# Performance work log

Measured on AMD Instinct MI355X. Metric: run time of the kernel, lower is better.

## Reference

```python
import jax, jax.numpy as jnp
import numpy as np

NUM_HEADS = 16


def setup_inputs() -> dict:
    key = jax.random.key(0)
    ks = jax.random.split(key, 5)
    S, B, N, C = 4, 2, 2048, 1024
    return {
        "x_all": jax.random.normal(ks[0], (S, B, N, C), dtype=jnp.float32),
        "w_qkv": jax.random.normal(ks[1], (C, 3 * C), dtype=jnp.float32) * (C ** -0.5),
        "b_qkv": jax.random.normal(ks[2], (3 * C,), dtype=jnp.float32) * 0.02,
        "w_proj": jax.random.normal(ks[3], (C, C), dtype=jnp.float32) * (C ** -0.5),
        "b_proj": jax.random.normal(ks[4], (C,), dtype=jnp.float32) * 0.02,
    }


def reference(x_all, w_qkv, b_qkv, w_proj, b_proj):
    # x_all: [S, B, N, C] -- S = cp_dim ring shards, each rank holds [B, N, C]
    S, B, N, C = x_all.shape
    H = NUM_HEADS
    D = C // H
    scale = 1.0 / np.sqrt(D).astype(np.float32)

    # same qkv projection on every rank
    qkv = (jnp.einsum("sbnc,ce->sbne", x_all, w_qkv) + b_qkv)
    qkv = qkv.reshape(S, B, N, 3, H, D)
    # rank 0's queries: [B, H, N, D]
    q = jnp.transpose(qkv[0, :, :, 0], (0, 2, 1, 3))
    # all shards' keys/values: [S, B, H, N, D]
    k = jnp.transpose(qkv[:, :, :, 1], (0, 1, 3, 2, 4))
    v = jnp.transpose(qkv[:, :, :, 2], (0, 1, 3, 2, 4))

    # ring loop: online softmax merge across KV shards (numerically stable
    # form of the source's exp(lse)-weighted average)
    attn_out, lse = None, None
    for s in range(S):
        scores = jnp.einsum("bhnd,bhmd->bhnm", q, k[s]) * scale  # [B,H,N,N]
        new_lse = jax.nn.logsumexp(scores, axis=-1)               # [B,H,N]
        probs = jnp.exp(scores - new_lse[..., None])
        new_out = jnp.einsum("bhnm,bhmd->bhnd", probs, v[s])      # [B,H,N,D]
        if attn_out is None:
            attn_out, lse = new_out, new_lse
        else:
            m = jnp.logaddexp(lse, new_lse)
            attn_out = (attn_out * jnp.exp(lse - m)[..., None]
                        + new_out * jnp.exp(new_lse - m)[..., None])
            lse = m

    # [B,H,N,D] -> [B,N,C]
    out = jnp.transpose(attn_out, (0, 2, 1, 3)).reshape(B, N, C)
    return out @ w_proj + b_proj
```

## Files before the change

kernel.cpp:

```cpp
#include <hip/hip_runtime.h>
#include <hip/hip_bf16.h>


typedef __bf16 bf16x8 __attribute__((ext_vector_type(8)));
typedef float v4f __attribute__((ext_vector_type(4)));

#if __has_builtin(__builtin_amdgcn_exp2f)
#define EXP2F(x) __builtin_amdgcn_exp2f(x)
#else
#define EXP2F(x) exp2f(x)
#endif

__device__ __forceinline__ float bf2f(unsigned short h) {
  union { unsigned int u; float f; } a; a.u = ((unsigned int)h) << 16; return a.f;
}
__device__ __forceinline__ unsigned short f2bf(float f) {
  union { float f; unsigned int u; } a; a.f = f;
  unsigned int u = a.u;
  unsigned int r = (u + 0x7fffu + ((u >> 16) & 1u)) >> 16;
  return (unsigned short)r;
}
__device__ __forceinline__ unsigned int pack2t(float a, float b) {
  union { float f; unsigned int u; } ua, ub; ua.f = a; ub.f = b;
  return (ua.u >> 16) | (ub.u & 0xffff0000u);
}
__device__ __forceinline__ bf16x8 ldfrag16(const unsigned short* p) {
  union { uint4 u; bf16x8 v; } x; x.u = *(const uint4*)p; return x.v;
}
__device__ __forceinline__ bf16x8 ones8() {
  union { unsigned short s[8]; bf16x8 v; } x;
#pragma unroll
  for (int i = 0; i < 8; i++) x.s[i] = 0x3F80;
  return x.v;
}
__device__ __forceinline__ void gld_lds16(const unsigned short* g, unsigned short* l) {
  __builtin_amdgcn_global_load_lds((__attribute__((address_space(1))) void*)g,
                                   (__attribute__((address_space(3))) void*)l, 16, 0, 0);
}

__global__ void detect_dtype(const unsigned short* __restrict__ x, int* flag) {
  __shared__ int cnt;
  if (threadIdx.x == 0) cnt = 0;
  __syncthreads();
  int sane = 0;
#pragma unroll
  for (int j = 0; j < 4; j++) {
    unsigned short v = x[2 * (threadIdx.x + 64 * j)];
    int e = (v >> 7) & 0xFF;
    if (e >= 90 && e <= 140) sane++;
  }
  atomicAdd(&cnt, sane);
  __syncthreads();
  if (threadIdx.x == 0) *flag = (cnt > 160) ? 0 : 1;
}

__global__ void conv_to_bf16(const void* __restrict__ in, unsigned short* __restrict__ out,
                             int n4, const int* __restrict__ flag) {
  int i = blockIdx.x * blockDim.x + threadIdx.x;
  if (i >= n4) return;
  if (*flag) {
    float4 v = ((const float4*)in)[i];
    ushort4 o;
    o.x = f2bf(v.x); o.y = f2bf(v.y); o.z = f2bf(v.z); o.w = f2bf(v.w);
    ((ushort4*)out)[i] = o;
  } else {
    ((ushort4*)out)[i] = ((const ushort4*)in)[i];
  }
}

__global__ void conv_bias(const void* __restrict__ bq_in, const void* __restrict__ bp_in,
                          unsigned short* __restrict__ bq, unsigned short* __restrict__ bp,
                          const int* __restrict__ flag) {
  int i = blockIdx.x * 256 + threadIdx.x;
  const void* in = (i < 768) ? bq_in : bp_in;
  unsigned short* out = (i < 768) ? bq : bp;
  int j = (i < 768) ? i : i - 768;
  if (*flag) {
    float4 v = ((const float4*)in)[j];
    ushort4 o;
    o.x = f2bf(v.x); o.y = f2bf(v.y); o.z = f2bf(v.z); o.w = f2bf(v.w);
    ((ushort4*)out)[j] = o;
  } else {
    ((ushort4*)out)[j] = ((const ushort4*)in)[j];
  }
}

__global__ void trans_both(const void* __restrict__ wqkv, const void* __restrict__ wproj,
                           unsigned short* __restrict__ wt1, unsigned short* __restrict__ wt2,
                           const int* __restrict__ flag) {
  __shared__ unsigned short t[32][33];
  int tx = threadIdx.x, ty = threadIdx.y;
  int bx = blockIdx.x;
  const void* in; unsigned short* out; int C, c0;
  if (bx < 96) { in = wqkv; out = wt1; C = 3072; c0 = bx * 32; }
  else         { in = wproj; out = wt2; C = 1024; c0 = (bx - 96) * 32; }
  const int R = 1024;
  int r0 = blockIdx.y * 32;
  int fp = *flag;
#pragma unroll
  for (int j = 0; j < 32; j += 8) {
    unsigned short v;
    if (fp) v = f2bf(((const float*)in)[(r0 + ty + j) * C + c0 + tx]);
    else    v = ((const unsigned short*)in)[(r0 + ty + j) * C + c0 + tx];
    t[ty + j][tx] = v;
  }
  __syncthreads();
#pragma unroll
  for (int j = 0; j < 32; j += 8) out[(c0 + ty + j) * R + r0 + tx] = t[tx][ty + j];
}

template <int MODE>
__launch_bounds__(256, 3)
__global__ void gemm_bt(const unsigned short* __restrict__ A,
                        const unsigned short* __restrict__ Bt,
                        const unsigned short* __restrict__ bias,
                        void* __restrict__ Cout,
                        int K, int ldc, const int* __restrict__ flag,
                        const unsigned short* Bt2, const unsigned short* bias2,
                        void* Cout2,
                        const unsigned short* Bt3, const unsigned short* bias3,
                        void* Cout3) {
  __shared__ unsigned short As[128 * 32];
  __shared__ unsigned short Bs[128 * 32];
  int tid = threadIdx.x;
  int w = tid >> 6, lane = tid & 63, col = lane & 15, quad = lane >> 4;
  int wm = w >> 1, wn = w & 1;
  const unsigned short* Bt_ = Bt;
  const unsigned short* bias_ = bias;
  void* Cout_ = Cout;
  bool isq = false, isv = false;
  int n0, m0;
  if constexpr (MODE == 4) {
    int id = blockIdx.x;
    int xcd = id & 7, t = id >> 3;
    n0 = (t & 7) * 128;
    int y = xcd * 36 + (t >> 3);
    if (y < 256) {
      m0 = (y >> 1) * 128;
      if (y & 1) { isv = true; Bt_ = Bt3; bias_ = bias3; Cout_ = Cout3; }
    } else {
      m0 = (y - 256) * 128;
      isq = true; Bt_ = Bt2; bias_ = bias2; Cout_ = Cout2;
    }
  } else {
    int id = blockIdx.x;
    int xcd = id & 7, t = id >> 3;
    n0 = (t & 7) * 128;
    m0 = (xcd * 4 + (t >> 3)) * 128;
  }
  int fp = 0;
  if constexpr (MODE == 2) fp = *flag;

  v4f acc[4][4];
#pragma unroll
  for (int i = 0; i < 4; i++)
#pragma unroll
    for (int j = 0; j < 4; j++) acc[i][j] = v4f{0.f, 0.f, 0.f, 0.f};

  int ra0 = tid >> 2, cc = tid & 3;
  const unsigned short* ga0 = &A[(m0 + ra0) * K + cc * 8];
  const unsigned short* ga1 = ga0 + 64 * K;
  const unsigned short* gb0 = &Bt_[(n0 + ra0) * K + cc * 8];
  const unsigned short* gb1 = gb0 + 64 * K;
  unsigned short* lA0 = &As[(w * 16) * 32];
  unsigned short* lA1 = &As[(64 + w * 16) * 32];
  unsigned short* lB0 = &Bs[(w * 16) * 32];
  unsigned short* lB1 = &Bs[(64 + w * 16) * 32];

  int niter = K >> 5;
  for (int it = 0; it < niter; it++) {
    __syncthreads();
    gld_lds16(ga0, lA0); gld_lds16(ga1, lA1);
    gld_lds16(gb0, lB0); gld_lds16(gb1, lB1);
    ga0 += 32; ga1 += 32; gb0 += 32; gb1 += 32;
    __syncthreads();
    bf16x8 af[4], bfr[4];
#pragma unroll
    for (int mi = 0; mi < 4; mi++) af[mi] = ldfrag16(&As[(wm * 64 + mi * 16 + col) * 32 + quad * 8]);
#pragma unroll
    for (int ni = 0; ni < 4; ni++) bfr[ni] = ldfrag16(&Bs[(wn * 64 + ni * 16 + col) * 32 + quad * 8]);
#pragma unroll
    for (int mi = 0; mi < 4; mi++)
#pragma unroll
      for (int ni = 0; ni < 4; ni++)
        acc[mi][ni] = __builtin_amdgcn_mfma_f32_16x16x32_bf16(af[mi], bfr[ni], acc[mi][ni], 0, 0, 0);
  }

  float bv[4];
#pragma unroll
  for (int ni = 0; ni < 4; ni++) bv[ni] = bf2f(bias_[n0 + wn * 64 + ni * 16 + col]);

  if (MODE == 4 && isv) {
    int rgb0 = m0 + wm * 64;
    int s = rgb0 >> 12, b = (rgb0 >> 11) & 1, n = rgb0 & 2047;
    int kvg0 = s * 2048 + n;
#pragma unroll
    for (int ni = 0; ni < 4; ni++) {
      int cg = n0 + wn * 64 + ni * 16 + col;
      int h = cg >> 6, d = cg & 63;
      unsigned short* rowp = &((unsigned short*)Cout_)[((b * 16 + h) * 64 + d) * 8192 + kvg0];
      float bvn = bv[ni];
#pragma unroll
      for (int r = 0; r < 4; r++) {
        ushort2 e, o2;
        e.x = f2bf(acc[0][ni][r] + bvn);
        e.y = f2bf(acc[2][ni][r] + bvn);
        o2.x = f2bf(acc[1][ni][r] + bvn);
        o2.y = f2bf(acc[3][ni][r] + bvn);
        *(ushort2*)&rowp[2 * (quad * 4 + r)] = e;
        *(ushort2*)&rowp[32 + 2 * (quad * 4 + r)] = o2;
      }
    }
  } else {
#pragma unroll
    for (int mi = 0; mi < 4; mi++)
#pragma unroll
      for (int ni = 0; ni < 4; ni++) {
        float vals[4];
#pragma unroll
        for (int r = 0; r < 4; r++) vals[r] = acc[mi][ni][r] + bv[ni];
        if constexpr (MODE == 4) {
          if (isq) {
#pragma unroll
            for (int r = 0; r < 4; r++) vals[r] *= 0.1803368801111601f;
          }
        }
        int rgb = m0 + wm * 64 + mi * 16 + quad * 4;
        int cg  = n0 + wn * 64 + ni * 16 + col;
        if constexpr (MODE == 4) {
          unsigned short* C = (unsigned short*)Cout_;
#pragma unroll
          for (int r = 0; r < 4; r++) C[(rgb + r) * ldc + cg] = f2bf(vals[r]);
        } else {
          if (fp) {
            float* C = (float*)Cout_;
#pragma unroll
            for (int r = 0; r < 4; r++) C[(rgb + r) * ldc + cg] = vals[r];
          } else {
            unsigned short* C = (unsigned short*)Cout_;
#pragma unroll
            for (int r = 0; r < 4; r++) C[(rgb + r) * ldc + cg] = f2bf(vals[r]);
          }
        }
      }
  }
}

__launch_bounds__(512, 4)
__global__ void attn_kernel(const unsigned short* __restrict__ qbuf,
                            const unsigned short* __restrict__ kbuf,
                            const unsigned short* __restrict__ vt,
                            float* __restrict__ po,
                            float* __restrict__ lbuf) {
  __shared__ unsigned short Ks[2][64 * 64];
  __shared__ unsigned short Vs[3][64 * 64];
  int tid = threadIdx.x;
  int w = tid >> 6, lane = tid & 63, col = lane & 15, quad = lane >> 4;
  int id = blockIdx.x;
  int xcd = id & 7, slot = id >> 3;
  int qt = slot & 7, gsub = slot >> 3;
  int g = gsub * 8 + xcd;
  int bh = g >> 1, half = g & 1;
  int b = bh >> 4, h = bh & 15;
  int q0 = qt * 256;

  bf16x8 aQ[2][2];
#pragma unroll
  for (int mj = 0; mj < 2; mj++)
#pragma unroll
    for (int kk = 0; kk < 2; kk++)
      aQ[mj][kk] = ldfrag16(&qbuf[(b * 2048 + q0 + w * 32 + mj * 16 + col) * 1024 +
                                  h * 64 + kk * 32 + quad * 8]);

  int r0 = tid >> 3, c0 = tid & 7;
  const unsigned short* kp = &kbuf[((half * 2) * 4096 + b * 2048 + r0) * 1024 + h * 64 + c0 * 8];
  const unsigned short* vp = &vt[(bh * 64 + r0) * 8192 + half * 4096 + c0 * 8];
  int sdst = r0 * 64 + 8 * (c0 ^ (r0 & 7));

  const bf16x8 vone = ones8();
  v4f o[2][4];
  v4f acc_l[2] = {v4f{0.f, 0.f, 0.f, 0.f}, v4f{0.f, 0.f, 0.f, 0.f}};
#pragma unroll
  for (int mj = 0; mj < 2; mj++)
#pragma unroll
    for (int di = 0; di < 4; di++) o[mj][di] = v4f{0.f, 0.f, 0.f, 0.f};

  {
    uint4 k0 = *(const uint4*)kp, v0 = *(const uint4*)vp;
    *(uint4*)&Ks[0][sdst] = k0;
    *(uint4*)&Vs[0][sdst] = v0;
  }
  kp += 64 * 1024; vp += 64;
  uint4 pk = *(const uint4*)kp, pv = *(const uint4*)vp;
  __syncthreads();

  bf16x8 aP[2][2];
  {
    v4f sc[4][2];
#pragma unroll
    for (int ni = 0; ni < 4; ni++)
#pragma unroll
      for (int mj = 0; mj < 2; mj++) sc[ni][mj] = v4f{0.f, 0.f, 0.f, 0.f};
#pragma unroll
    for (int kk = 0; kk < 2; kk++) {
      bf16x8 aK[4];
#pragma unroll
      for (int ni = 0; ni < 4; ni++) {
        int row = ni * 16 + col;
        aK[ni] = ldfrag16(&Ks[0][row * 64 + 8 * ((kk * 4 + quad) ^ (col & 7))]);
      }
#pragma unroll
      for (int ni = 0; ni < 4; ni++)
#pragma unroll
        for (int mj = 0; mj < 2; mj++)
          sc[ni][mj] = __builtin_amdgcn_mfma_f32_16x16x32_bf16(aK[ni], aQ[mj][kk], sc[ni][mj], 0, 0, 0);
    }
#pragma unroll
    for (int ni = 0; ni < 4; ni++)
#pragma unroll
      for (int mj = 0; mj < 2; mj++)
#pragma unroll
        for (int r = 0; r < 4; r++) sc[ni][mj][r] = EXP2F(sc[ni][mj][r]);
#pragma unroll
    for (int mj = 0; mj < 2; mj++)
#pragma unroll
      for (int kk = 0; kk < 2; kk++) {
        union { unsigned int d[4]; bf16x8 v; } u;
#pragma unroll
        for (int t = 0; t < 4; t++)
          u.d[t] = pack2t(sc[kk][mj][t], sc[kk + 2][mj][t]);
        aP[mj][kk] = u.v;
      }
  }
  *(uint4*)&Ks[1][sdst] = pk;
  *(uint4*)&Vs[1][sdst] = pv;
  __syncthreads();

  const unsigned short* vprev = Vs[0];
  const unsigned short* vcur  = Vs[1];
  const unsigned short* vnext = Vs[2];

  for (int t = 1; t < 64; t++) {
    const unsigned short* kcur = Ks[t & 1];
    unsigned short* knxt = (unsigned short*)Ks[(t + 1) & 1];
    if (t < 63) {
      int kstep = (((t + 1) & 31) == 0) ? (2048 + 64) * 1024 : 64 * 1024;
      kp += kstep; vp += 64;
      pk = *(const uint4*)kp; pv = *(const uint4*)vp;
    }

    v4f sc[4][2];
#pragma unroll
    for (int ni = 0; ni < 4; ni++)
#pragma unroll
      for (int mj = 0; mj < 2; mj++) sc[ni][mj] = v4f{0.f, 0.f, 0.f, 0.f};
#pragma unroll
    for (int kk = 0; kk < 2; kk++) {
      bf16x8 aK[4];
#pragma unroll
      for (int ni = 0; ni < 4; ni++) {
        int row = ni * 16 + col;
        aK[ni] = ldfrag16(&kcur[row * 64 + 8 * ((kk * 4 + quad) ^ (col & 7))]);
      }
#pragma unroll
      for (int ni = 0; ni < 4; ni++)
#pragma unroll
        for (int mj = 0; mj < 2; mj++)
          sc[ni][mj] = __builtin_amdgcn_mfma_f32_16x16x32_bf16(aK[ni], aQ[mj][kk], sc[ni][mj], 0, 0, 0);
    }

#pragma unroll
    for (int kk = 0; kk < 2; kk++) {
#pragma unroll
      for (int mj = 0; mj < 2; mj++)
        acc_l[mj] = __builtin_amdgcn_mfma_f32_16x16x32_bf16(aP[mj][kk], vone, acc_l[mj], 0, 0, 0);
      bf16x8 bV[4];
#pragma unroll
      for (int di = 0; di < 4; di++) {
        int row = di * 16 + col;
        bV[di] = ldfrag16(&vprev[row * 64 + 8 * ((kk * 4 + quad) ^ (col & 7))]);
      }
#pragma unroll
      for (int mj = 0; mj < 2; mj++)
#pragma unroll
        for (int di = 0; di < 4; di++)
          o[mj][di] = __builtin_amdgcn_mfma_f32_16x16x32_bf16(aP[mj][kk], bV[di], o[mj][di], 0, 0, 0);
    }

#pragma unroll
    for (int ni = 0; ni < 4; ni++)
#pragma unroll
      for (int mj = 0; mj < 2; mj++)
#pragma unroll
        for (int r = 0; r < 4; r++) sc[ni][mj][r] = EXP2F(sc[ni][mj][r]);
    bf16x8 aPn[2][2];
#pragma unroll
    for (int mj = 0; mj < 2; mj++)
#pragma unroll
      for (int kk = 0; kk < 2; kk++) {
        union { unsigned int d[4]; bf16x8 v; } u;
#pragma unroll
        for (int tt = 0; tt < 4; tt++)
          u.d[tt] = pack2t(sc[kk][mj][tt], sc[kk + 2][mj][tt]);
        aPn[mj][kk] = u.v;
      }

    if (t < 63) {
      *(uint4*)&knxt[sdst] = pk;
      *(uint4*)&((unsigned short*)vnext)[sdst] = pv;
    }

    __syncthreads();

#pragma unroll
    for (int mj = 0; mj < 2; mj++)
#pragma unroll
      for (int kk = 0; kk < 2; kk++) aP[mj][kk] = aPn[mj][kk];
    const unsigned short* vt_ = vprev;
    vprev = vcur; vcur = vnext; vnext = vt_;
  }

#pragma unroll
  for (int kk = 0; kk < 2; kk++) {
#pragma unroll
    for (int mj = 0; mj < 2; mj++)
      acc_l[mj] = __builtin_amdgcn_mfma_f32_16x16x32_bf16(aP[mj][kk], vone, acc_l[mj], 0, 0, 0);
    bf16x8 bV[4];
#pragma unroll
    for (int di = 0; di < 4; di++) {
      int row = di * 16 + col;
      bV[di] = ldfrag16(&vprev[row * 64 + 8 * ((kk * 4 + quad) ^ (col & 7))]);
    }
#pragma unroll
    for (int mj = 0; mj < 2; mj++)
#pragma unroll
      for (int di = 0; di < 4; di++)
        o[mj][di] = __builtin_amdgcn_mfma_f32_16x16x32_bf16(aP[mj][kk], bV[di], o[mj][di], 0, 0, 0);
  }

  float* pb = po + half * 4194304;
#pragma unroll
  for (int mj = 0; mj < 2; mj++)
#pragma unroll
    for (int r = 0; r < 4; r++) {
      int n = q0 + w * 32 + mj * 16 + quad * 4 + r;
      if (col == 0) lbuf[half * 65536 + (b * 16 + h) * 2048 + n] = acc_l[mj][r];
#pragma unroll
      for (int di = 0; di < 4; di++) {
        int c = h * 64 + di * 16 + col;
        pb[(b * 2048 + n) * 1024 + c] = o[mj][di][r];
      }
    }
}

__global__ void merge_halves(const float* __restrict__ po, const float* __restrict__ lbuf,
                             unsigned short* __restrict__ attn) {
  int i = blockIdx.x * 256 + threadIdx.x;
  int r = i >> 8, c4 = i & 255;
  float l = lbuf[((r >> 11) * 16 + (c4 >> 4)) * 2048 + (r & 2047)] +
            lbuf[65536 + ((r >> 11) * 16 + (c4 >> 4)) * 2048 + (r & 2047)];
  float inv = 1.f / l;
  float4 a = ((const float4*)po)[i];
  float4 b = ((const float4*)po)[1048576 + i];
  ushort4 o;
  o.x = f2bf((a.x + b.x) * inv); o.y = f2bf((a.y + b.y) * inv);
  o.z = f2bf((a.z + b.z) * inv); o.w = f2bf((a.w + b.w) * inv);
  ((ushort4*)attn)[i] = o;
}

extern "C" void kernel_launch(void* const* d_in, const int* in_sizes, int n_in,
                              void* d_out, int out_size, void* d_ws, size_t ws_size,
                              hipStream_t stream) {
  const void* x      = d_in[0];
  const void* w_qkv  = d_in[1];
  const void* b_qkv  = d_in[2];
  const void* w_proj = d_in[3];
  const void* b_proj = d_in[4];

  char* ws = (char*)d_ws;
  unsigned short* xb   = (unsigned short*)(ws);
  unsigned short* kk   = (unsigned short*)(ws + 33554432);
  unsigned short* vt   = (unsigned short*)(ws + 67108864);
  unsigned short* q0b  = (unsigned short*)(ws + 100663296);
  unsigned short* attn = (unsigned short*)(ws + 109051904);
  unsigned short* wt1  = (unsigned short*)(ws + 117440512);
  unsigned short* wt2  = (unsigned short*)(ws + 123731968);
  unsigned short* bq   = (unsigned short*)(ws + 125829120);
  unsigned short* bp   = (unsigned short*)(ws + 125835264);
  int* flag            = (int*)(ws + 125837312);
  float* po   = (float*)xb;
  float* lbuf = (float*)wt1;

  detect_dtype<<<1, 64, 0, stream>>>((const unsigned short*)x, flag);

  conv_to_bf16<<<16384, 256, 0, stream>>>(x, xb, 4194304, flag);
  conv_bias<<<4, 256, 0, stream>>>(b_qkv, b_proj, bq, bp, flag);
  trans_both<<<dim3(128, 32), dim3(32, 8), 0, stream>>>(w_qkv, w_proj, wt1, wt2, flag);

  gemm_bt<4><<<2304, 256, 0, stream>>>(xb, wt1 + 1024 * 1024, bq + 1024, kk,
                                       1024, 1024, flag,
                                       wt1, bq, q0b,
                                       wt1 + 2048 * 1024, bq + 2048, vt);

  attn_kernel<<<512, 512, 0, stream>>>(q0b, kk, vt, po, lbuf);
  merge_halves<<<4096, 256, 0, stream>>>(po, lbuf, attn);

  gemm_bt<2><<<256, 256, 0, stream>>>(attn, wt2, bp, d_out,
                                      1024, 1024, flag,
                                      nullptr, nullptr, nullptr,
                                      nullptr, nullptr, nullptr);
}
```

Measured before the change: 291.6 us.

## Halve attention block size to 4 waves and double grid to 1024 blocks

```diff
diff --git a/kernel.cpp b/kernel.cpp
--- a/kernel.cpp
+++ b/kernel.cpp
@@ -246,7 +246,7 @@
   }
 }
 
-__launch_bounds__(512, 4)
+__launch_bounds__(256, 4)
 __global__ void attn_kernel(const unsigned short* __restrict__ qbuf,
                             const unsigned short* __restrict__ kbuf,
                             const unsigned short* __restrict__ vt,
@@ -258,11 +258,11 @@
   int w = tid >> 6, lane = tid & 63, col = lane & 15, quad = lane >> 4;
   int id = blockIdx.x;
   int xcd = id & 7, slot = id >> 3;
-  int qt = slot & 7, gsub = slot >> 3;
+  int qt = slot & 15, gsub = slot >> 4;
   int g = gsub * 8 + xcd;
   int bh = g >> 1, half = g & 1;
   int b = bh >> 4, h = bh & 15;
-  int q0 = qt * 256;
+  int q0 = qt * 128;
 
   bf16x8 aQ[2][2];
 #pragma unroll
@@ -272,10 +272,13 @@
       aQ[mj][kk] = ldfrag16(&qbuf[(b * 2048 + q0 + w * 32 + mj * 16 + col) * 1024 +
                                   h * 64 + kk * 32 + quad * 8]);
 
-  int r0 = tid >> 3, c0 = tid & 7;
-  const unsigned short* kp = &kbuf[((half * 2) * 4096 + b * 2048 + r0) * 1024 + h * 64 + c0 * 8];
-  const unsigned short* vp = &vt[(bh * 64 + r0) * 8192 + half * 4096 + c0 * 8];
-  int sdst = r0 * 64 + 8 * (c0 ^ (r0 & 7));
+  int r0 = tid >> 2, c0 = tid & 3;
+  const unsigned short* kp0 = &kbuf[((half * 2) * 4096 + b * 2048 + r0) * 1024 + h * 64 + c0 * 8];
+  const unsigned short* kp1 = kp0 + 32;
+  const unsigned short* vp0 = &vt[(bh * 64 + r0) * 8192 + half * 4096 + c0 * 8];
+  const unsigned short* vp1 = vp0 + 32;
+  int sd0 = r0 * 64 + 8 * (c0 ^ (r0 & 7));
+  int sd1 = r0 * 64 + 8 * ((c0 + 4) ^ (r0 & 7));
 
   const bf16x8 vone = ones8();
   v4f o[2][4];
@@ -286,12 +289,14 @@
     for (int di = 0; di < 4; di++) o[mj][di] = v4f{0.f, 0.f, 0.f, 0.f};
 
   {
-    uint4 k0 = *(const uint4*)kp, v0 = *(const uint4*)vp;
-    *(uint4*)&Ks[0][sdst] = k0;
-    *(uint4*)&Vs[0][sdst] = v0;
-  }
-  kp += 64 * 1024; vp += 64;
-  uint4 pk = *(const uint4*)kp, pv = *(const uint4*)vp;
+    uint4 ka = *(const uint4*)kp0, kb = *(const uint4*)kp1;
+    uint4 va = *(const uint4*)vp0, vb = *(const uint4*)vp1;
+    *(uint4*)&Ks[0][sd0] = ka; *(uint4*)&Ks[0][sd1] = kb;
+    *(uint4*)&Vs[0][sd0] = va; *(uint4*)&Vs[0][sd1] = vb;
+  }
+  kp0 += 64 * 1024; kp1 += 64 * 1024; vp0 += 64; vp1 += 64;
+  uint4 pk0 = *(const uint4*)kp0, pk1 = *(const uint4*)kp1;
+  uint4 pv0 = *(const uint4*)vp0, pv1 = *(const uint4*)vp1;
   __syncthreads();
 
   bf16x8 aP[2][2];
@@ -332,8 +337,8 @@
         aP[mj][kk] = u.v;
       }
   }
-  *(uint4*)&Ks[1][sdst] = pk;
-  *(uint4*)&Vs[1][sdst] = pv;
+  *(uint4*)&Ks[1][sd0] = pk0; *(uint4*)&Ks[1][sd1] = pk1;
+  *(uint4*)&Vs[1][sd0] = pv0; *(uint4*)&Vs[1][sd1] = pv1;
   __syncthreads();
 
   const unsigned short* vprev = Vs[0];
@@ -345,8 +350,9 @@
     unsigned short* knxt = (unsigned short*)Ks[(t + 1) & 1];
     if (t < 63) {
       int kstep = (((t + 1) & 31) == 0) ? (2048 + 64) * 1024 : 64 * 1024;
-      kp += kstep; vp += 64;
-      pk = *(const uint4*)kp; pv = *(const uint4*)vp;
+      kp0 += kstep; kp1 += kstep; vp0 += 64; vp1 += 64;
+      pk0 = *(const uint4*)kp0; pk1 = *(const uint4*)kp1;
+      pv0 = *(const uint4*)vp0; pv1 = *(const uint4*)vp1;
     }
 
     v4f sc[4][2];
@@ -406,8 +412,9 @@
       }
 
     if (t < 63) {
-      *(uint4*)&knxt[sdst] = pk;
-      *(uint4*)&((unsigned short*)vnext)[sdst] = pv;
+      *(uint4*)&knxt[sd0] = pk0; *(uint4*)&knxt[sd1] = pk1;
+      *(uint4*)&((unsigned short*)vnext)[sd0] = pv0;
+      *(uint4*)&((unsigned short*)vnext)[sd1] = pv1;
     }
 
     __syncthreads();
@@ -502,7 +509,7 @@
                                        wt1, bq, q0b,
                                        wt1 + 2048 * 1024, bq + 2048, vt);
 
-  attn_kernel<<<512, 512, 0, stream>>>(q0b, kk, vt, po, lbuf);
+  attn_kernel<<<1024, 256, 0, stream>>>(q0b, kk, vt, po, lbuf);
   merge_halves<<<4096, 256, 0, stream>>>(po, lbuf, attn);
 
   gemm_bt<2><<<256, 256, 0, stream>>>(attn, wt2, bp, d_out,
```

New measurement: 304.5 us. +4.4%, slower.
